# Performance work log

Measured on AMD Instinct MI355X. Metric: run time of the kernel, lower is better.

The kernel has to match this reference:

```python
import jax, jax.numpy as jnp
import numpy as np

B = 4096
D_IN = 1024
HIDDEN = [1024, 512, 256]
NUM_DOMAINS = 8


def _glorot(key, shape):
    fan_in, fan_out = shape[-2], shape[-1]
    std = np.sqrt(2.0 / (fan_in + fan_out)).astype(np.float32)
    return jax.random.normal(key, shape, dtype=jnp.float32) * std


def setup_inputs() -> dict:
    key = jax.random.key(0)
    keys = jax.random.split(key, 16)
    dims = [D_IN] + HIDDEN  # per-layer (in, out) = (dims[i], dims[i+1])
    inp = {
        "x": jax.random.normal(keys[0], (B, D_IN), dtype=jnp.float32),
        "indicator": jax.random.randint(keys[1], (B,), 0, NUM_DOMAINS, dtype=jnp.int32),
    }
    for i in range(len(HIDDEN)):
        inp[f"sk{i}"] = _glorot(keys[2 + i], (dims[i], dims[i + 1]))
        inp[f"sb{i}"] = jnp.zeros((dims[i + 1],), dtype=jnp.float32)
        # per-domain kernels stacked on leading domain axis: (D, in, out)
        inp[f"dk{i}"] = _glorot(keys[6 + i], (NUM_DOMAINS, dims[i], dims[i + 1]))
        inp[f"db{i}"] = jnp.zeros((NUM_DOMAINS, dims[i + 1]), dtype=jnp.float32)
    return inp


def reference(x, indicator, sk0, sb0, dk0, db0, sk1, sb1, dk1, db1, sk2, sb2, dk2, db2):
    shared_k = [sk0, sk1, sk2]
    shared_b = [sb0, sb1, sb2]
    domain_k = [dk0, dk1, dk2]
    domain_b = [db0, db1, db2]
    D = dk0.shape[0]
    # Replicate input across all domains: [B, D, d_in] (source computes every domain stack)
    h = jnp.broadcast_to(x[:, None, :], (x.shape[0], D, x.shape[1]))
    for sk, sb, dk, db in zip(shared_k, shared_b, domain_k, domain_b):
        w_eff = sk[None, :, :] * dk          # [D, in, out]  fused shared*domain weights
        b_eff = sb[None, :] + db             # [D, out]
        h = jnp.einsum('bdi,dio->bdo', h, w_eff) + b_eff[None, :, :]
        h = jax.nn.relu(h)                   # all layers use 'relu' (no output_activation)
    one_hot = jax.nn.one_hot(indicator, D, dtype=h.dtype)  # [B, D]
    return jnp.einsum('bdo,bd->bo', h, one_hot)
```

## Files before the change

kernel.cpp:

```cpp
#include <hip/hip_runtime.h>

#define NROWS 4096
#define NDOM 8

typedef short short8 __attribute__((ext_vector_type(8)));
typedef float floatx4 __attribute__((ext_vector_type(4)));
typedef unsigned short ushort8v __attribute__((ext_vector_type(8)));

__device__ __forceinline__ unsigned short f2bf(float f) {
    union { float f; unsigned u; } v; v.f = f;
    unsigned r = v.u + 0x7FFFu + ((v.u >> 16) & 1u);
    return (unsigned short)(r >> 16);
}

__device__ __forceinline__ void dma16(const void* g, void* l) {
    __builtin_amdgcn_global_load_lds(
        (const __attribute__((address_space(1))) unsigned*)g,
        (__attribute__((address_space(3))) unsigned*)l, 16, 0, 0);
}


template <int K, int N>
__device__ __forceinline__ void weff_tile(const float* __restrict__ sk,
                                          const float* __restrict__ dk,
                                          unsigned short* __restrict__ wt,
                                          unsigned short* __restrict__ lds,
                                          int local) {
    const int d = local & 7;
    const int rest = local >> 3;
    const int k0 = (rest & (K / 256 - 1)) * 256;
    const int n0 = (rest / (K / 256)) * 64;
    const int t = threadIdx.x;

    const int n = t & 63;
    const int kg = (t >> 6) * 64;
#pragma unroll
    for (int c8 = 0; c8 < 8; ++c8) {
        const int kb = k0 + kg + c8 * 8;
        unsigned short wb[8];
#pragma unroll
        for (int i = 0; i < 8; ++i) {
            int k = kb + i;
            wb[i] = f2bf(sk[(size_t)k * N + n0 + n] * dk[((size_t)d * K + k) * N + n0 + n]);
        }
        int ch = (kg + c8 * 8) >> 3;
        int phys = ch ^ (n & 31);
        *(ushort8v*)&lds[n * 256 + phys * 8] = *(ushort8v*)wb;
    }
    __syncthreads();

#pragma unroll
    for (int it = 0; it < 4; ++it) {
        const int nn = (t >> 4) + it * 16;
        const int c = t & 15;
        ushort8v a = *(ushort8v*)&lds[nn * 256 + ((2 * c) ^ (nn & 31)) * 8];
        ushort8v b = *(ushort8v*)&lds[nn * 256 + ((2 * c + 1) ^ (nn & 31)) * 8];
        unsigned short* dst = wt + ((size_t)d * N + n0 + nn) * K + k0 + c * 16;
        *(ushort8v*)dst = a;
        *(ushort8v*)(dst + 8) = b;
    }
}

__global__ void precompute_kernel(const float* __restrict__ x,
                                  const int* __restrict__ ind,
                                  const float* __restrict__ sk0, const float* __restrict__ dk0,
                                  const float* __restrict__ sk1, const float* __restrict__ dk1,
                                  const float* __restrict__ sk2, const float* __restrict__ dk2,
                                  unsigned short* __restrict__ xb,
                                  unsigned short* __restrict__ w0t,
                                  unsigned short* __restrict__ w1t,
                                  unsigned short* __restrict__ w2t,
                                  int* __restrict__ offsets,
                                  int* __restrict__ rowidx) {
    __shared__ unsigned short wtile[64 * 256];
    __shared__ unsigned short cnt[256][NDOM];
    __shared__ int base[256][NDOM];
    __shared__ int dom_total[NDOM];
    __shared__ int dom_off[NDOM + 1];

    const int b = blockIdx.x;
    const int t = threadIdx.x;

    if (b < 256) {
#pragma unroll
        for (int pass = 0; pass < 8; ++pass) {
            int row = b * 16 + pass * 2 + (t >> 7);
            int ch = t & 127;
            const float* src = x + (size_t)row * 1024 + ch * 8;
            floatx4 v0 = *(const floatx4*)src;
            floatx4 v1 = *(const floatx4*)(src + 4);
            unsigned short o[8];
            o[0] = f2bf(v0[0]); o[1] = f2bf(v0[1]); o[2] = f2bf(v0[2]); o[3] = f2bf(v0[3]);
            o[4] = f2bf(v1[0]); o[5] = f2bf(v1[1]); o[6] = f2bf(v1[2]); o[7] = f2bf(v1[3]);
            *(ushort8v*)(xb + (size_t)row * 1024 + ch * 8) = *(ushort8v*)o;
        }
    } else if (b < 256 + 512) {
        weff_tile<1024, 1024>(sk0, dk0, w0t, wtile, b - 256);
    } else if (b < 256 + 512 + 256) {
        weff_tile<1024, 512>(sk1, dk1, w1t, wtile, b - (256 + 512));
    } else if (b < 256 + 512 + 256 + 64) {
        weff_tile<512, 256>(sk2, dk2, w2t, wtile, b - (256 + 512 + 256));
    } else {
        int myind[16];
#pragma unroll
        for (int i = 0; i < 16; ++i) myind[i] = ind[t * 16 + i];
        unsigned short c[NDOM];
#pragma unroll
        for (int d = 0; d < NDOM; ++d) c[d] = 0;
#pragma unroll
        for (int i = 0; i < 16; ++i) c[myind[i]]++;
#pragma unroll
        for (int d = 0; d < NDOM; ++d) cnt[t][d] = c[d];
        __syncthreads();
        if (t < NDOM) {
            int acc = 0;
            for (int ch = 0; ch < 256; ++ch) { base[ch][t] = acc; acc += cnt[ch][t]; }
            dom_total[t] = acc;
        }
        __syncthreads();
        if (t == 0) {
            int acc = 0;
            for (int d = 0; d < NDOM; ++d) { dom_off[d] = acc; acc += dom_total[d]; }
            dom_off[NDOM] = acc;
        }
        __syncthreads();
        int pos[NDOM];
#pragma unroll
        for (int d = 0; d < NDOM; ++d) pos[d] = dom_off[d] + base[t][d];
#pragma unroll
        for (int i = 0; i < 16; ++i) {
            int dm = myind[i];
            rowidx[pos[dm]++] = t * 16 + i;
        }
        if (t <= NDOM) offsets[t] = dom_off[t];
    }
}

template <int FM, int FN, int MSLOTS, int K, int N, bool GATHER, bool SCATTER>
__launch_bounds__(256)
__global__ void star_gemm(const unsigned short* __restrict__ Ab,
                          const unsigned short* __restrict__ Wt,
                          const float* __restrict__ sb,
                          const float* __restrict__ db,
                          float* __restrict__ OutF,
                          unsigned short* __restrict__ OutB,
                          const int* __restrict__ offsets,
                          const int* __restrict__ rowidx) {
    constexpr int BM = 32 * FM;
    constexpr int BN = 32 * FN;
    constexpr int NK = K / 64;
    constexpr int AI = BM / 32;
    constexpr int WI = BN / 32;

    __shared__ __align__(128) unsigned short As[2][BM * 64];
    __shared__ __align__(128) unsigned short Ws[2][BN * 64];

    const int gid = blockIdx.x;
    const int d = gid & 7;
    const int mslot = (gid >> 3) % MSLOTS;
    const int n0 = (gid / (8 * MSLOTS)) * BN;

    const int bstart = offsets[d];
    const int bend = offsets[d + 1];
    const int bsize = bend - bstart;

    const int tid = threadIdx.x;
    const int lane = tid & 63;
    const int w = tid >> 6;
    const int wy = w >> 1;
    const int wx = w & 1;
    const int lm = lane & 15;
    const int quad = lane >> 4;

    const int lrow = lane >> 3;
    const int phys = lane & 7;

    float bias[FN];
#pragma unroll
    for (int j = 0; j < FN; ++j) {
        int n = n0 + wx * FN * 16 + j * 16 + lm;
        bias[j] = sb[n] + db[d * N + n];
    }

    const unsigned short* wsrc[WI];
#pragma unroll
    for (int j = 0; j < WI; ++j) {
        int nr0 = (w * WI + j) * 8;
        int nn = nr0 + lrow;
        int ch = phys ^ (nn & 7);
        wsrc[j] = Wt + ((size_t)d * N + n0 + nn) * K + ch * 8;
    }

    for (int mt = mslot; mt * BM < bsize; mt += MSLOTS) {
        const int row_start = bstart + mt * BM;

        const unsigned short* asrc[AI];
#pragma unroll
        for (int j = 0; j < AI; ++j) {
            int m0 = (w * AI + j) * 8;
            int mm = m0 + lrow;
            int ch = phys ^ (mm & 7);
            int p = row_start + mm; if (p >= bend) p = bend - 1;
            int src = GATHER ? rowidx[p] : p;
            asrc[j] = Ab + (size_t)src * K + ch * 8;
        }

        auto dma_tiles = [&](int kt, int buf) {
            const int k0 = kt * 64;
#pragma unroll
            for (int j = 0; j < AI; ++j)
                dma16(asrc[j] + k0, &As[buf][(w * AI + j) * 512]);
#pragma unroll
            for (int j = 0; j < WI; ++j)
                dma16(wsrc[j] + k0, &Ws[buf][(w * WI + j) * 512]);
        };

        floatx4 acc[FM][FN];
#pragma unroll
        for (int i = 0; i < FM; ++i)
#pragma unroll
            for (int j = 0; j < FN; ++j) acc[i][j] = floatx4{0.f, 0.f, 0.f, 0.f};

        dma_tiles(0, 0);
        for (int kt = 0; kt < NK; ++kt) {
            const int buf = kt & 1;
            __syncthreads();

            short8 av[2][FM], wv[2][FN];
#pragma unroll
            for (int kk = 0; kk < 2; ++kk) {
#pragma unroll
                for (int i = 0; i < FM; ++i) {
                    int m = wy * FM * 16 + i * 16 + lm;
                    int pc = (kk * 4 + quad) ^ (m & 7);
                    av[kk][i] = *(const short8*)&As[buf][m * 64 + pc * 8];
                }
#pragma unroll
                for (int j = 0; j < FN; ++j) {
                    int n = wx * FN * 16 + j * 16 + lm;
                    int pc = (kk * 4 + quad) ^ (n & 7);
                    wv[kk][j] = *(const short8*)&Ws[buf][n * 64 + pc * 8];
                }
            }
            if (kt + 1 < NK) dma_tiles(kt + 1, 1 - buf);
#pragma unroll
            for (int kk = 0; kk < 2; ++kk)
#pragma unroll
                for (int i = 0; i < FM; ++i)
#pragma unroll
                    for (int j = 0; j < FN; ++j)
                        acc[i][j] = __builtin_amdgcn_mfma_f32_16x16x32_bf16(
                            av[kk][i], wv[kk][j], acc[i][j], 0, 0, 0);
        }

#pragma unroll
        for (int i = 0; i < FM; ++i) {
#pragma unroll
            for (int rg = 0; rg < 4; ++rg) {
                int m = wy * FM * 16 + i * 16 + quad * 4 + rg;
                int p = row_start + m;
                if (p < bend) {
                    if constexpr (SCATTER) {
                        int orow = rowidx[p];
#pragma unroll
                        for (int j = 0; j < FN; ++j) {
                            int n = n0 + wx * FN * 16 + j * 16 + lm;
                            float v = acc[i][j][rg] + bias[j];
                            OutF[(size_t)orow * N + n] = v > 0.f ? v : 0.f;
                        }
                    } else {
#pragma unroll
                        for (int j = 0; j < FN; ++j) {
                            int n = n0 + wx * FN * 16 + j * 16 + lm;
                            float v = acc[i][j][rg] + bias[j];
                            OutB[(size_t)p * N + n] = f2bf(v > 0.f ? v : 0.f);
                        }
                    }
                }
            }
        }
    }
}

extern "C" void kernel_launch(void* const* d_in, const int* in_sizes, int n_in,
                              void* d_out, int out_size, void* d_ws, size_t ws_size,
                              hipStream_t stream) {
    const float* x = (const float*)d_in[0];
    const int* ind = (const int*)d_in[1];
    const float* sk0 = (const float*)d_in[2];
    const float* sb0 = (const float*)d_in[3];
    const float* dk0 = (const float*)d_in[4];
    const float* db0 = (const float*)d_in[5];
    const float* sk1 = (const float*)d_in[6];
    const float* sb1 = (const float*)d_in[7];
    const float* dk1 = (const float*)d_in[8];
    const float* db1 = (const float*)d_in[9];
    const float* sk2 = (const float*)d_in[10];
    const float* sb2 = (const float*)d_in[11];
    const float* dk2 = (const float*)d_in[12];
    const float* db2 = (const float*)d_in[13];
    float* out = (float*)d_out;

    char* ws = (char*)d_ws;
    int* offsets = (int*)ws;
    int* rowidx = (int*)(ws + 256);
    unsigned short* xb  = (unsigned short*)(ws + 32768);
    unsigned short* h1  = xb + (size_t)NROWS * 1024;
    unsigned short* h2  = h1 + (size_t)NROWS * 1024;
    unsigned short* w0t = h2 + (size_t)NROWS * 512;
    unsigned short* w1t = w0t + (size_t)NDOM * 1024 * 1024;
    unsigned short* w2t = w1t + (size_t)NDOM * 512 * 1024;

    precompute_kernel<<<256 + 512 + 256 + 64 + 1, 256, 0, stream>>>(
        x, ind, sk0, dk0, sk1, dk1, sk2, dk2, xb, w0t, w1t, w2t, offsets, rowidx);

    star_gemm<2, 2, 8, 1024, 1024, true, false><<<1024, 256, 0, stream>>>(
        xb, w0t, sb0, db0, nullptr, h1, offsets, rowidx);
    star_gemm<2, 2, 8, 1024, 512, false, false><<<512, 256, 0, stream>>>(
        h1, w1t, sb1, db1, nullptr, h2, offsets, rowidx);
    star_gemm<1, 2, 16, 512, 256, false, true><<<512, 256, 0, stream>>>(
        h2, w2t, sb2, db2, out, nullptr, offsets, rowidx);
}
```

Before: 187.6 us.

## Replace LDS-staged GEMM with per-wave direct global loads into registers

The grouped GEMM no longer stages A and W tiles through shared memory with global_load_lds double buffering and block barriers. Each wave now owns an independent output tile, loads MFMA fragments straight from global memory into registers with a three-deep prefetch, and needs no __syncthreads. Launch configs and per-wave tile sizes change to match, with fewer blocks per layer. The cost is that waves no longer share operand tiles, so global and L2 traffic rises, and the strided 16-byte loads coalesce less well.

```diff
diff --git a/kernel.cpp b/kernel.cpp
--- a/kernel.cpp
+++ b/kernel.cpp
@@ -11,12 +11,6 @@
     union { float f; unsigned u; } v; v.f = f;
     unsigned r = v.u + 0x7FFFu + ((v.u >> 16) & 1u);
     return (unsigned short)(r >> 16);
-}
-
-__device__ __forceinline__ void dma16(const void* g, void* l) {
-    __builtin_amdgcn_global_load_lds(
-        (const __attribute__((address_space(1))) unsigned*)g,
-        (__attribute__((address_space(3))) unsigned*)l, 16, 0, 0);
 }
 
 
@@ -137,7 +131,7 @@
 }
 
 template <int FM, int FN, int MSLOTS, int K, int N, bool GATHER, bool SCATTER>
-__launch_bounds__(256)
+__launch_bounds__(256, 1)
 __global__ void star_gemm(const unsigned short* __restrict__ Ab,
                           const unsigned short* __restrict__ Wt,
                           const float* __restrict__ sb,
@@ -146,132 +140,96 @@
                           unsigned short* __restrict__ OutB,
                           const int* __restrict__ offsets,
                           const int* __restrict__ rowidx) {
-    constexpr int BM = 32 * FM;
-    constexpr int BN = 32 * FN;
-    constexpr int NK = K / 64;
-    constexpr int AI = BM / 32;
-    constexpr int WI = BN / 32;
-
-    __shared__ __align__(128) unsigned short As[2][BM * 64];
-    __shared__ __align__(128) unsigned short Ws[2][BN * 64];
+    constexpr int TM = FM * 16;
+    constexpr int TN = FN * 16;
+    constexpr int NS = K / 32;
 
     const int gid = blockIdx.x;
+    const int w = threadIdx.x >> 6;
+    const int lane = threadIdx.x & 63;
+    const int lm = lane & 15;
+    const int quad = lane >> 4;
+
     const int d = gid & 7;
-    const int mslot = (gid >> 3) % MSLOTS;
-    const int n0 = (gid / (8 * MSLOTS)) * BN;
+    const int rest = (gid >> 3) * 4 + w;
+    const int mslot = rest % MSLOTS;
+    const int n0 = (rest / MSLOTS) * TN;
 
     const int bstart = offsets[d];
     const int bend = offsets[d + 1];
     const int bsize = bend - bstart;
 
-    const int tid = threadIdx.x;
-    const int lane = tid & 63;
-    const int w = tid >> 6;
-    const int wy = w >> 1;
-    const int wx = w & 1;
-    const int lm = lane & 15;
-    const int quad = lane >> 4;
-
-    const int lrow = lane >> 3;
-    const int phys = lane & 7;
-
     float bias[FN];
+    const unsigned short* wp[FN];
 #pragma unroll
     for (int j = 0; j < FN; ++j) {
-        int n = n0 + wx * FN * 16 + j * 16 + lm;
+        int n = n0 + j * 16 + lm;
         bias[j] = sb[n] + db[d * N + n];
-    }
-
-    const unsigned short* wsrc[WI];
-#pragma unroll
-    for (int j = 0; j < WI; ++j) {
-        int nr0 = (w * WI + j) * 8;
-        int nn = nr0 + lrow;
-        int ch = phys ^ (nn & 7);
-        wsrc[j] = Wt + ((size_t)d * N + n0 + nn) * K + ch * 8;
-    }
-
-    for (int mt = mslot; mt * BM < bsize; mt += MSLOTS) {
-        const int row_start = bstart + mt * BM;
-
-        const unsigned short* asrc[AI];
-#pragma unroll
-        for (int j = 0; j < AI; ++j) {
-            int m0 = (w * AI + j) * 8;
-            int mm = m0 + lrow;
-            int ch = phys ^ (mm & 7);
-            int p = row_start + mm; if (p >= bend) p = bend - 1;
+        wp[j] = Wt + ((size_t)d * N + n) * K + quad * 8;
+    }
+
+    for (int mt = mslot; mt * TM < bsize; mt += MSLOTS) {
+        const int row_start = bstart + mt * TM;
+
+        const unsigned short* ap[FM];
+#pragma unroll
+        for (int i = 0; i < FM; ++i) {
+            int p = row_start + i * 16 + lm;
+            if (p >= bend) p = bend - 1;
             int src = GATHER ? rowidx[p] : p;
-            asrc[j] = Ab + (size_t)src * K + ch * 8;
-        }
-
-        auto dma_tiles = [&](int kt, int buf) {
-            const int k0 = kt * 64;
-#pragma unroll
-            for (int j = 0; j < AI; ++j)
-                dma16(asrc[j] + k0, &As[buf][(w * AI + j) * 512]);
-#pragma unroll
-            for (int j = 0; j < WI; ++j)
-                dma16(wsrc[j] + k0, &Ws[buf][(w * WI + j) * 512]);
+            ap[i] = Ab + (size_t)src * K + quad * 8;
+        }
+
+        floatx4 acc[FM][FN];
+#pragma unroll
+        for (int i = 0; i < FM; ++i)
+#pragma unroll
+            for (int j = 0; j < FN; ++j) acc[i][j] = floatx4{0.f, 0.f, 0.f, 0.f};
+
+        short8 ab[3][FM], wb[3][FN];
+        auto load = [&](int s, int buf) {
+#pragma unroll
+            for (int i = 0; i < FM; ++i)
+                ab[buf][i] = *(const short8*)(ap[i] + s * 32);
+#pragma unroll
+            for (int j = 0; j < FN; ++j)
+                wb[buf][j] = *(const short8*)(wp[j] + s * 32);
         };
 
-        floatx4 acc[FM][FN];
-#pragma unroll
-        for (int i = 0; i < FM; ++i)
-#pragma unroll
-            for (int j = 0; j < FN; ++j) acc[i][j] = floatx4{0.f, 0.f, 0.f, 0.f};
-
-        dma_tiles(0, 0);
-        for (int kt = 0; kt < NK; ++kt) {
-            const int buf = kt & 1;
-            __syncthreads();
-
-            short8 av[2][FM], wv[2][FN];
-#pragma unroll
-            for (int kk = 0; kk < 2; ++kk) {
-#pragma unroll
-                for (int i = 0; i < FM; ++i) {
-                    int m = wy * FM * 16 + i * 16 + lm;
-                    int pc = (kk * 4 + quad) ^ (m & 7);
-                    av[kk][i] = *(const short8*)&As[buf][m * 64 + pc * 8];
-                }
-#pragma unroll
-                for (int j = 0; j < FN; ++j) {
-                    int n = wx * FN * 16 + j * 16 + lm;
-                    int pc = (kk * 4 + quad) ^ (n & 7);
-                    wv[kk][j] = *(const short8*)&Ws[buf][n * 64 + pc * 8];
-                }
-            }
-            if (kt + 1 < NK) dma_tiles(kt + 1, 1 - buf);
-#pragma unroll
-            for (int kk = 0; kk < 2; ++kk)
-#pragma unroll
-                for (int i = 0; i < FM; ++i)
-#pragma unroll
-                    for (int j = 0; j < FN; ++j)
-                        acc[i][j] = __builtin_amdgcn_mfma_f32_16x16x32_bf16(
-                            av[kk][i], wv[kk][j], acc[i][j], 0, 0, 0);
+        load(0, 0);
+        load(1, 1);
+        load(2, 2);
+#pragma unroll
+        for (int s = 0; s < NS; ++s) {
+            const int buf = s % 3;
+#pragma unroll
+            for (int i = 0; i < FM; ++i)
+#pragma unroll
+                for (int j = 0; j < FN; ++j)
+                    acc[i][j] = __builtin_amdgcn_mfma_f32_16x16x32_bf16(
+                        ab[buf][i], wb[buf][j], acc[i][j], 0, 0, 0);
+            if (s + 3 < NS) load(s + 3, buf);
         }
 
 #pragma unroll
         for (int i = 0; i < FM; ++i) {
 #pragma unroll
             for (int rg = 0; rg < 4; ++rg) {
-                int m = wy * FM * 16 + i * 16 + quad * 4 + rg;
+                int m = i * 16 + quad * 4 + rg;
                 int p = row_start + m;
                 if (p < bend) {
                     if constexpr (SCATTER) {
                         int orow = rowidx[p];
 #pragma unroll
                         for (int j = 0; j < FN; ++j) {
-                            int n = n0 + wx * FN * 16 + j * 16 + lm;
+                            int n = n0 + j * 16 + lm;
                             float v = acc[i][j][rg] + bias[j];
                             OutF[(size_t)orow * N + n] = v > 0.f ? v : 0.f;
                         }
                     } else {
 #pragma unroll
                         for (int j = 0; j < FN; ++j) {
-                            int n = n0 + wx * FN * 16 + j * 16 + lm;
+                            int n = n0 + j * 16 + lm;
                             float v = acc[i][j][rg] + bias[j];
                             OutB[(size_t)p * N + n] = f2bf(v > 0.f ? v : 0.f);
                         }
@@ -314,10 +272,10 @@
     precompute_kernel<<<256 + 512 + 256 + 64 + 1, 256, 0, stream>>>(
         x, ind, sk0, dk0, sk1, dk1, sk2, dk2, xb, w0t, w1t, w2t, offsets, rowidx);
 
-    star_gemm<2, 2, 8, 1024, 1024, true, false><<<1024, 256, 0, stream>>>(
+    star_gemm<4, 4, 8, 1024, 1024, true, false><<<256, 256, 0, stream>>>(
         xb, w0t, sb0, db0, nullptr, h1, offsets, rowidx);
-    star_gemm<2, 2, 8, 1024, 512, false, false><<<512, 256, 0, stream>>>(
+    star_gemm<2, 4, 16, 1024, 512, false, false><<<256, 256, 0, stream>>>(
         h1, w1t, sb1, db1, nullptr, h2, offsets, rowidx);
-    star_gemm<1, 2, 16, 512, 256, false, true><<<512, 256, 0, stream>>>(
+    star_gemm<2, 2, 16, 512, 256, false, true><<<256, 256, 0, stream>>>(
         h2, w2t, sb2, db2, out, nullptr, offsets, rowidx);
 }
```

Result: slower. 262.9 us (+40.1%).

## Overlap layer-1/2 weight prep with layer-0 GEMM and widen GEMM tiles

Applied to the files above, without the earlier changes.

Splits the precompute kernel so only x conversion, layer-0 weight fusion and domain bucketing run first. The layer-1 and layer-2 fused-weight tiles are built in a combined kernel that shares the launch with the layer-0 GEMM blocks, so they fill idle CUs alongside it. The weight-fusion loads now use coalesced float4 reads instead of strided scalar loads, and the first two GEMMs use wider N tiles (FN=4) with half as many blocks. The trade-off is more LDS per block and fewer blocks in flight, plus heterogeneous blocks within one launch that can be unevenly balanced.

```diff
diff --git a/kernel.cpp b/kernel.cpp
--- a/kernel.cpp
+++ b/kernel.cpp
@@ -18,7 +18,6 @@
         (const __attribute__((address_space(1))) unsigned*)g,
         (__attribute__((address_space(3))) unsigned*)l, 16, 0, 0);
 }
-
 
 template <int K, int N>
 __device__ __forceinline__ void weff_tile(const float* __restrict__ sk,
@@ -32,20 +31,21 @@
     const int n0 = (rest / (K / 256)) * 64;
     const int t = threadIdx.x;
 
-    const int n = t & 63;
-    const int kg = (t >> 6) * 64;
-#pragma unroll
-    for (int c8 = 0; c8 < 8; ++c8) {
-        const int kb = k0 + kg + c8 * 8;
-        unsigned short wb[8];
-#pragma unroll
-        for (int i = 0; i < 8; ++i) {
-            int k = kb + i;
-            wb[i] = f2bf(sk[(size_t)k * N + n0 + n] * dk[((size_t)d * K + k) * N + n0 + n]);
-        }
-        int ch = (kg + c8 * 8) >> 3;
-        int phys = ch ^ (n & 31);
-        *(ushort8v*)&lds[n * 256 + phys * 8] = *(ushort8v*)wb;
+    const int q = t & 15;
+    const int kr = t >> 4;
+    const int ke = kr & 7;
+#pragma unroll
+    for (int pass = 0; pass < 16; ++pass) {
+        const int krel = pass * 16 + kr;
+        const int k = k0 + krel;
+        floatx4 s = *(const floatx4*)(sk + (size_t)k * N + n0 + q * 4);
+        floatx4 dd = *(const floatx4*)(dk + ((size_t)d * K + k) * N + n0 + q * 4);
+        const int ch = krel >> 3;
+#pragma unroll
+        for (int c = 0; c < 4; ++c) {
+            int n = q * 4 + c;
+            lds[n * 256 + (ch ^ (n & 31)) * 8 + ke] = f2bf(s[c] * dd[c]);
+        }
     }
     __syncthreads();
 
@@ -61,17 +61,158 @@
     }
 }
 
-__global__ void precompute_kernel(const float* __restrict__ x,
-                                  const int* __restrict__ ind,
-                                  const float* __restrict__ sk0, const float* __restrict__ dk0,
-                                  const float* __restrict__ sk1, const float* __restrict__ dk1,
-                                  const float* __restrict__ sk2, const float* __restrict__ dk2,
-                                  unsigned short* __restrict__ xb,
-                                  unsigned short* __restrict__ w0t,
-                                  unsigned short* __restrict__ w1t,
-                                  unsigned short* __restrict__ w2t,
-                                  int* __restrict__ offsets,
-                                  int* __restrict__ rowidx) {
+template <int FM, int FN, int MSLOTS, int K, int N, bool GATHER, bool SCATTER>
+__device__ __forceinline__ void gemm_body(char* smem, int gid,
+                                          const unsigned short* __restrict__ Ab,
+                                          const unsigned short* __restrict__ Wt,
+                                          const float* __restrict__ sb,
+                                          const float* __restrict__ db,
+                                          float* __restrict__ OutF,
+                                          unsigned short* __restrict__ OutB,
+                                          const int* __restrict__ offsets,
+                                          const int* __restrict__ rowidx) {
+    constexpr int BM = 32 * FM;
+    constexpr int BN = 32 * FN;
+    constexpr int NK = K / 64;
+    constexpr int AI = BM / 32;
+    constexpr int WI = BN / 32;
+
+    unsigned short* As = (unsigned short*)smem;
+    unsigned short* Ws = As + 2 * BM * 64;
+
+    const int d = gid & 7;
+    const int mslot = (gid >> 3) % MSLOTS;
+    const int n0 = ((gid >> 3) / MSLOTS) * BN;
+
+    const int bstart = offsets[d];
+    const int bend = offsets[d + 1];
+    const int bsize = bend - bstart;
+
+    const int tid = threadIdx.x;
+    const int lane = tid & 63;
+    const int w = tid >> 6;
+    const int wy = w >> 1;
+    const int wx = w & 1;
+    const int lm = lane & 15;
+    const int quad = lane >> 4;
+
+    const int lrow = lane >> 3;
+    const int phys = lane & 7;
+
+    float bias[FN];
+#pragma unroll
+    for (int j = 0; j < FN; ++j) {
+        int n = n0 + wx * FN * 16 + j * 16 + lm;
+        bias[j] = sb[n] + db[d * N + n];
+    }
+
+    const unsigned short* wsrc[WI];
+#pragma unroll
+    for (int j = 0; j < WI; ++j) {
+        int nr0 = (w * WI + j) * 8;
+        int nn = nr0 + lrow;
+        int ch = phys ^ (nn & 7);
+        wsrc[j] = Wt + ((size_t)d * N + n0 + nn) * K + ch * 8;
+    }
+
+    for (int mt = mslot; mt * BM < bsize; mt += MSLOTS) {
+        const int row_start = bstart + mt * BM;
+
+        const unsigned short* asrc[AI];
+#pragma unroll
+        for (int j = 0; j < AI; ++j) {
+            int m0 = (w * AI + j) * 8;
+            int mm = m0 + lrow;
+            int ch = phys ^ (mm & 7);
+            int p = row_start + mm; if (p >= bend) p = bend - 1;
+            int src = GATHER ? rowidx[p] : p;
+            asrc[j] = Ab + (size_t)src * K + ch * 8;
+        }
+
+        auto dma_tiles = [&](int kt, int buf) {
+            const int k0 = kt * 64;
+#pragma unroll
+            for (int j = 0; j < AI; ++j)
+                dma16(asrc[j] + k0, As + buf * BM * 64 + (w * AI + j) * 512);
+#pragma unroll
+            for (int j = 0; j < WI; ++j)
+                dma16(wsrc[j] + k0, Ws + buf * BN * 64 + (w * WI + j) * 512);
+        };
+
+        floatx4 acc[FM][FN];
+#pragma unroll
+        for (int i = 0; i < FM; ++i)
+#pragma unroll
+            for (int j = 0; j < FN; ++j) acc[i][j] = floatx4{0.f, 0.f, 0.f, 0.f};
+
+        dma_tiles(0, 0);
+        for (int kt = 0; kt < NK; ++kt) {
+            const int buf = kt & 1;
+            __syncthreads();
+
+            short8 av[2][FM], wv[2][FN];
+#pragma unroll
+            for (int kk = 0; kk < 2; ++kk) {
+#pragma unroll
+                for (int i = 0; i < FM; ++i) {
+                    int m = wy * FM * 16 + i * 16 + lm;
+                    int pc = (kk * 4 + quad) ^ (m & 7);
+                    av[kk][i] = *(const short8*)&As[buf * BM * 64 + m * 64 + pc * 8];
+                }
+#pragma unroll
+                for (int j = 0; j < FN; ++j) {
+                    int n = wx * FN * 16 + j * 16 + lm;
+                    int pc = (kk * 4 + quad) ^ (n & 7);
+                    wv[kk][j] = *(const short8*)&Ws[buf * BN * 64 + n * 64 + pc * 8];
+                }
+            }
+            if (kt + 1 < NK) dma_tiles(kt + 1, 1 - buf);
+#pragma unroll
+            for (int kk = 0; kk < 2; ++kk)
+#pragma unroll
+                for (int i = 0; i < FM; ++i)
+#pragma unroll
+                    for (int j = 0; j < FN; ++j)
+                        acc[i][j] = __builtin_amdgcn_mfma_f32_16x16x32_bf16(
+                            av[kk][i], wv[kk][j], acc[i][j], 0, 0, 0);
+        }
+
+#pragma unroll
+        for (int i = 0; i < FM; ++i) {
+#pragma unroll
+            for (int rg = 0; rg < 4; ++rg) {
+                int m = wy * FM * 16 + i * 16 + quad * 4 + rg;
+                int p = row_start + m;
+                if (p < bend) {
+                    if constexpr (SCATTER) {
+                        int orow = rowidx[p];
+#pragma unroll
+                        for (int j = 0; j < FN; ++j) {
+                            int n = n0 + wx * FN * 16 + j * 16 + lm;
+                            float v = acc[i][j][rg] + bias[j];
+                            OutF[(size_t)orow * N + n] = v > 0.f ? v : 0.f;
+                        }
+                    } else {
+#pragma unroll
+                        for (int j = 0; j < FN; ++j) {
+                            int n = n0 + wx * FN * 16 + j * 16 + lm;
+                            float v = acc[i][j][rg] + bias[j];
+                            OutB[(size_t)p * N + n] = f2bf(v > 0.f ? v : 0.f);
+                        }
+                    }
+                }
+            }
+        }
+    }
+}
+
+__global__ void pre0_kernel(const float* __restrict__ x,
+                            const int* __restrict__ ind,
+                            const float* __restrict__ sk0, const float* __restrict__ dk0,
+                            unsigned short* __restrict__ xb,
+                            unsigned short* __restrict__ w0t,
+                            int* __restrict__ offsets,
+                            int* __restrict__ rowidx) {
     __shared__ unsigned short wtile[64 * 256];
     __shared__ unsigned short cnt[256][NDOM];
     __shared__ int base[256][NDOM];
@@ -96,10 +237,6 @@
         }
     } else if (b < 256 + 512) {
         weff_tile<1024, 1024>(sk0, dk0, w0t, wtile, b - 256);
-    } else if (b < 256 + 512 + 256) {
-        weff_tile<1024, 512>(sk1, dk1, w1t, wtile, b - (256 + 512));
-    } else if (b < 256 + 512 + 256 + 64) {
-        weff_tile<512, 256>(sk2, dk2, w2t, wtile, b - (256 + 512 + 256));
     } else {
         int myind[16];
 #pragma unroll
@@ -133,6 +270,29 @@
             rowidx[pos[dm]++] = t * 16 + i;
         }
         if (t <= NDOM) offsets[t] = dom_off[t];
+    }
+}
+
+__launch_bounds__(256)
+__global__ void combo_kernel(const unsigned short* __restrict__ xb,
+                             const unsigned short* __restrict__ w0t,
+                             const float* __restrict__ sb0, const float* __restrict__ db0,
+                             unsigned short* __restrict__ h1,
+                             const float* __restrict__ sk1, const float* __restrict__ dk1,
+                             const float* __restrict__ sk2, const float* __restrict__ dk2,
+                             unsigned short* __restrict__ w1t,
+                             unsigned short* __restrict__ w2t,
+                             const int* __restrict__ offsets,
+                             const int* __restrict__ rowidx) {
+    __shared__ __align__(16) char smem[49152];
+    const int b = blockIdx.x;
+    if (b < 512) {
+        gemm_body<2, 4, 8, 1024, 1024, true, false>(
+            smem, b, xb, w0t, sb0, db0, nullptr, h1, offsets, rowidx);
+    } else if (b < 768) {
+        weff_tile<1024, 512>(sk1, dk1, w1t, (unsigned short*)smem, b - 512);
+    } else {
+        weff_tile<512, 256>(sk2, dk2, w2t, (unsigned short*)smem, b - 768);
     }
 }
 
@@ -146,140 +306,9 @@
                           unsigned short* __restrict__ OutB,
                           const int* __restrict__ offsets,
                           const int* __restrict__ rowidx) {
-    constexpr int BM = 32 * FM;
-    constexpr int BN = 32 * FN;
-    constexpr int NK = K / 64;
-    constexpr int AI = BM / 32;
-    constexpr int WI = BN / 32;
-
-    __shared__ __align__(128) unsigned short As[2][BM * 64];
-    __shared__ __align__(128) unsigned short Ws[2][BN * 64];
-
-    const int gid = blockIdx.x;
-    const int d = gid & 7;
-    const int mslot = (gid >> 3) % MSLOTS;
-    const int n0 = (gid / (8 * MSLOTS)) * BN;
-
-    const int bstart = offsets[d];
-    const int bend = offsets[d + 1];
-    const int bsize = bend - bstart;
-
-    const int tid = threadIdx.x;
-    const int lane = tid & 63;
-    const int w = tid >> 6;
-    const int wy = w >> 1;
-    const int wx = w & 1;
-    const int lm = lane & 15;
-    const int quad = lane >> 4;
-
-    const int lrow = lane >> 3;
-    const int phys = lane & 7;
-
-    float bias[FN];
-#pragma unroll
-    for (int j = 0; j < FN; ++j) {
-        int n = n0 + wx * FN * 16 + j * 16 + lm;
-        bias[j] = sb[n] + db[d * N + n];
-    }
-
-    const unsigned short* wsrc[WI];
-#pragma unroll
-    for (int j = 0; j < WI; ++j) {
-        int nr0 = (w * WI + j) * 8;
-        int nn = nr0 + lrow;
-        int ch = phys ^ (nn & 7);
-        wsrc[j] = Wt + ((size_t)d * N + n0 + nn) * K + ch * 8;
-    }
-
-    for (int mt = mslot; mt * BM < bsize; mt += MSLOTS) {
-        const int row_start = bstart + mt * BM;
-
-        const unsigned short* asrc[AI];
-#pragma unroll
-        for (int j = 0; j < AI; ++j) {
-            int m0 = (w * AI + j) * 8;
-            int mm = m0 + lrow;
-            int ch = phys ^ (mm & 7);
-            int p = row_start + mm; if (p >= bend) p = bend - 1;
-            int src = GATHER ? rowidx[p] : p;
-            asrc[j] = Ab + (size_t)src * K + ch * 8;
-        }
-
-        auto dma_tiles = [&](int kt, int buf) {
-            const int k0 = kt * 64;
-#pragma unroll
-            for (int j = 0; j < AI; ++j)
-                dma16(asrc[j] + k0, &As[buf][(w * AI + j) * 512]);
-#pragma unroll
-            for (int j = 0; j < WI; ++j)
-                dma16(wsrc[j] + k0, &Ws[buf][(w * WI + j) * 512]);
-        };
-
-        floatx4 acc[FM][FN];
-#pragma unroll
-        for (int i = 0; i < FM; ++i)
-#pragma unroll
-            for (int j = 0; j < FN; ++j) acc[i][j] = floatx4{0.f, 0.f, 0.f, 0.f};
-
-        dma_tiles(0, 0);
-        for (int kt = 0; kt < NK; ++kt) {
-            const int buf = kt & 1;
-            __syncthreads();
-
-            short8 av[2][FM], wv[2][FN];
-#pragma unroll
-            for (int kk = 0; kk < 2; ++kk) {
-#pragma unroll
-                for (int i = 0; i < FM; ++i) {
-                    int m = wy * FM * 16 + i * 16 + lm;
-                    int pc = (kk * 4 + quad) ^ (m & 7);
-                    av[kk][i] = *(const short8*)&As[buf][m * 64 + pc * 8];
-                }
-#pragma unroll
-                for (int j = 0; j < FN; ++j) {
-                    int n = wx * FN * 16 + j * 16 + lm;
-                    int pc = (kk * 4 + quad) ^ (n & 7);
-                    wv[kk][j] = *(const short8*)&Ws[buf][n * 64 + pc * 8];
-                }
-            }
-            if (kt + 1 < NK) dma_tiles(kt + 1, 1 - buf);
-#pragma unroll
-            for (int kk = 0; kk < 2; ++kk)
-#pragma unroll
-                for (int i = 0; i < FM; ++i)
-#pragma unroll
-                    for (int j = 0; j < FN; ++j)
-                        acc[i][j] = __builtin_amdgcn_mfma_f32_16x16x32_bf16(
-                            av[kk][i], wv[kk][j], acc[i][j], 0, 0, 0);
-        }
-
-#pragma unroll
-        for (int i = 0; i < FM; ++i) {
-#pragma unroll
-            for (int rg = 0; rg < 4; ++rg) {
-                int m = wy * FM * 16 + i * 16 + quad * 4 + rg;
-                int p = row_start + m;
-                if (p < bend) {
-                    if constexpr (SCATTER) {
-                        int orow = rowidx[p];
-#pragma unroll
-                        for (int j = 0; j < FN; ++j) {
-                            int n = n0 + wx * FN * 16 + j * 16 + lm;
-                            float v = acc[i][j][rg] + bias[j];
-                            OutF[(size_t)orow * N + n] = v > 0.f ? v : 0.f;
-                        }
-                    } else {
-#pragma unroll
-                        for (int j = 0; j < FN; ++j) {
-                            int n = n0 + wx * FN * 16 + j * 16 + lm;
-                            float v = acc[i][j][rg] + bias[j];
-                            OutB[(size_t)p * N + n] = f2bf(v > 0.f ? v : 0.f);
-                        }
-                    }
-                }
-            }
-        }
-    }
+    __shared__ __align__(16) char smem[(2 * FM * 32 * 64 + 2 * FN * 32 * 64) * 2];
+    gemm_body<FM, FN, MSLOTS, K, N, GATHER, SCATTER>(
+        smem, blockIdx.x, Ab, Wt, sb, db, OutF, OutB, offsets, rowidx);
 }
 
 extern "C" void kernel_launch(void* const* d_in, const int* in_sizes, int n_in,
@@ -311,12 +340,13 @@
     unsigned short* w1t = w0t + (size_t)NDOM * 1024 * 1024;
     unsigned short* w2t = w1t + (size_t)NDOM * 512 * 1024;
 
-    precompute_kernel<<<256 + 512 + 256 + 64 + 1, 256, 0, stream>>>(
-        x, ind, sk0, dk0, sk1, dk1, sk2, dk2, xb, w0t, w1t, w2t, offsets, rowidx);
-
-    star_gemm<2, 2, 8, 1024, 1024, true, false><<<1024, 256, 0, stream>>>(
-        xb, w0t, sb0, db0, nullptr, h1, offsets, rowidx);
-    star_gemm<2, 2, 8, 1024, 512, false, false><<<512, 256, 0, stream>>>(
+    pre0_kernel<<<769, 256, 0, stream>>>(x, ind, sk0, dk0, xb, w0t, offsets, rowidx);
+
+    combo_kernel<<<832, 256, 0, stream>>>(xb, w0t, sb0, db0, h1,
+                                          sk1, dk1, sk2, dk2, w1t, w2t,
+                                          offsets, rowidx);
+
+    star_gemm<2, 4, 8, 1024, 512, false, false><<<256, 256, 0, stream>>>(
         h1, w1t, sb1, db1, nullptr, h2, offsets, rowidx);
     star_gemm<1, 2, 16, 512, 256, false, true><<<512, 256, 0, stream>>>(
         h2, w2t, sb2, db2, out, nullptr, offsets, rowidx);
```

Result: slower. 197.0 us (+5.0%).
